# Kernel optimization log

Hardware: AMD Instinct MI355X
Metric: run time of the kernel (lower is better)

## Reference

```python
import jax, jax.numpy as jnp
import numpy as np

NB, T, N, C = 8, 8, 6890, 128
CLASS_NUM = 7
D_SUM = 512
PCADIM = 64
V = 7702  # garment template vertex count
EPS = 1e-5


def setup_inputs() -> dict:
    key = jax.random.key(0)
    ks = jax.random.split(key, 12)
    f = lambda k, s: jax.random.normal(k, s, dtype=jnp.float32)
    return {
        "x": f(ks[0], (NB, T, N, 3)),
        "sem_logits": f(ks[1], (NB * T, N, CLASS_NUM)),
        "feature": f(ks[2], (NB * T, C, N)),
        "garment_summary": f(ks[3], (NB, T, D_SUM)),
        "W1": f(ks[4], (128, D_SUM)) * 0.02, "b1": jnp.zeros((128,), jnp.float32),
        "g1": jnp.ones((128,), jnp.float32), "be1": jnp.zeros((128,), jnp.float32),
        "rm1": jnp.zeros((128,), jnp.float32), "rv1": jnp.ones((128,), jnp.float32),
        "W2": f(ks[5], (64, 128)) * 0.02, "b2": jnp.zeros((64,), jnp.float32),
        "g2": jnp.ones((64,), jnp.float32), "be2": jnp.zeros((64,), jnp.float32),
        "rm2": jnp.zeros((64,), jnp.float32), "rv2": jnp.ones((64,), jnp.float32),
        "W3": f(ks[6], (PCADIM, 64)) * 0.02, "b3": jnp.zeros((PCADIM,), jnp.float32),
        "pca_comp": f(ks[7], (PCADIM, V * 3)) * 0.02,
        "pca_mean": f(ks[8], (V * 3,)) * 0.02,
        "pca_scale": jnp.abs(f(ks[9], (V * 3,))) + 0.5,
        "garment_label": 1,
        "n": N // 4,
    }


def _segmentation_gather(x, sem_logits, feature, garment_label, n):
    # Vectorized form of the per-sample boolean-mask select / truncate / zero-pad loop.
    # x: [B,N,3]; feature: [B,C,N]; sem_logits: [B,N,K]
    feat = jnp.swapaxes(feature, 1, 2)                     # [B,N,C]
    labels = jnp.argmax(sem_logits, axis=2)                # [B,N] (detached in original)
    mask = labels == garment_label                         # [B,N]
    count = mask.sum(axis=1)                               # [B]
    # stable argsort puts selected (mask=True -> key False=0) indices first, in order
    order = jnp.argsort(jnp.logical_not(mask), axis=1)[:, :n]   # [B,n]
    valid = (jnp.arange(n)[None, :] < count[:, None]).astype(x.dtype)  # [B,n]
    gv = jnp.take_along_axis(x, order[:, :, None], axis=1) * valid[:, :, None]
    gf = jnp.take_along_axis(feat, order[:, :, None], axis=1) * valid[:, :, None]
    return gv, gf


def reference(x, sem_logits, feature, garment_summary, W1, b1, g1, be1, rm1, rv1,
              W2, b2, g2, be2, rm2, rv2, W3, b3, pca_comp, pca_mean, pca_scale,
              garment_label, n):
    nbatch, t = x.shape[0], x.shape[1]
    xf = x.reshape(nbatch * t, -1, 3)
    garment_v, garment_f = _segmentation_gather(xf, sem_logits, feature, garment_label, n)

    # PCAEncoder: 1x1 Conv1d over a length-1 sequence == linear layers; BN in eval mode
    def bn(h, g, be, rm, rv):
        return (h - rm) * jax.lax.rsqrt(rv + EPS) * g + be

    gs = garment_summary.max(axis=1)                       # [nbatch, 512] (max over T)
    h = jax.nn.relu(bn(gs @ W1.T + b1, g1, be1, rm1, rv1))
    h = jax.nn.relu(bn(h @ W2.T + b2, g2, be2, rm2, rv2))
    coeff = h @ W3.T + b3                                  # [nbatch, PCADIM]

    # PCA_inverse_transform
    tpose = ((coeff @ pca_comp) + pca_mean) * pca_scale
    tpose = tpose.reshape(coeff.shape[0], -1, 3)           # [nbatch, V, 3]
    return garment_v, garment_f, coeff, tpose
```

## Files before the change

kernel.cpp:

```cpp
#include <hip/hip_runtime.h>

#define NBATCH   8
#define TT       8
#define NPTS     6890
#define KCLS     7
#define CCH      128
#define BSAMP    64
#define NOUT     1722
#define DSUM     512
#define PCADIM   64
#define V3       23106
#define EPSBN    1e-5f

#define NW       108
#define PCH      64
#define LDSP     129
#define CPG      6
#define NGRP     18
#define K4B      91
#define NGATHER  (BSAMP * NGRP)

#define OFF_GV     0
#define OFF_GF     (BSAMP * NOUT * 3)
#define OFF_COEFF  (OFF_GF + BSAMP * NOUT * CCH)
#define OFF_TPOSE  (OFF_COEFF + NBATCH * PCADIM)

__global__ __launch_bounds__(256) void k_prep(
    const float* __restrict__ logits,
    const int*   __restrict__ d_label,
    const float* __restrict__ x,
    unsigned long long* __restrict__ ws_mask,
    float* __restrict__ gv,
    int*   __restrict__ ws_spref,
    int*   __restrict__ ws_count,
    const float* __restrict__ gsum,
    const float* __restrict__ W1, const float* __restrict__ b1,
    const float* __restrict__ g1, const float* __restrict__ be1,
    const float* __restrict__ rm1, const float* __restrict__ rv1,
    const float* __restrict__ W2, const float* __restrict__ b2,
    const float* __restrict__ g2, const float* __restrict__ be2,
    const float* __restrict__ rm2, const float* __restrict__ rv2,
    const float* __restrict__ W3, const float* __restrict__ b3,
    float* __restrict__ coeff_out, float* __restrict__ coeff_ws)
{
    const int tid = threadIdx.x;

    if (blockIdx.x < BSAMP) {
        const int b = blockIdx.x;
        const int label = d_label[0];
        __shared__ unsigned long long smask[NW];
        __shared__ int spref[NW + 1];

        const float* lb = logits + (size_t)b * NPTS * KCLS;
        #pragma unroll 1
        for (int r = 0; r < 27; ++r) {
            const int i = r * 256 + tid;
            bool sel = false;
            if (i < NPTS) {
                const float* p = lb + (size_t)i * KCLS;
                float best = p[0]; int bi = 0;
                #pragma unroll
                for (int k = 1; k < KCLS; ++k) {
                    float v = p[k];
                    if (v > best) { best = v; bi = k; }
                }
                sel = (bi == label);
            }
            const unsigned long long m = __ballot(sel);
            if ((tid & 63) == 0) {
                const int w = r * 4 + (tid >> 6);
                if (w < NW) smask[w] = m;
            }
        }
        __syncthreads();

        if (tid == 0) {
            int run = 0;
            for (int w = 0; w < NW; ++w) { spref[w] = run; run += __popcll(smask[w]); }
            spref[NW] = run;
            ws_count[b] = run < NOUT ? run : NOUT;
        }
        __syncthreads();
        if (tid < NW) {
            ws_mask [b * NW + tid] = smask[tid];
            ws_spref[b * NW + tid] = spref[tid];
        }

        const float* xb = x + (size_t)b * NPTS * 3;
        for (int i = tid; i < NPTS; i += 256) {
            const int w = i >> 6, lb6 = i & 63;
            const unsigned long long m = smask[w];
            if ((m >> lb6) & 1ull) {
                const int pos = spref[w] + __popcll(m & ((1ull << lb6) - 1ull));
                if (pos < NOUT) {
                    const size_t go = ((size_t)b * NOUT + pos) * 3;
                    gv[go + 0] = xb[(size_t)i * 3 + 0];
                    gv[go + 1] = xb[(size_t)i * 3 + 1];
                    gv[go + 2] = xb[(size_t)i * 3 + 2];
                }
            }
        }

        int cnt = spref[NW]; if (cnt > NOUT) cnt = NOUT;
        for (int j = cnt + tid; j < NOUT; j += 256) {
            float* gp = gv + ((size_t)b * NOUT + j) * 3;
            gp[0] = 0.f; gp[1] = 0.f; gp[2] = 0.f;
        }
    } else {
        const int s    = blockIdx.x - BSAMP;
        const int lane = tid & 63;
        const int wv   = tid >> 6;

        __shared__ float gs[DSUM];
        __shared__ float h1[128];
        __shared__ float h2[64];

        for (int d = tid; d < DSUM; d += 256) {
            const float* p = gsum + ((size_t)s * TT) * DSUM + d;
            float m = p[0];
            #pragma unroll
            for (int t = 1; t < TT; ++t) m = fmaxf(m, p[(size_t)t * DSUM]);
            gs[d] = m;
        }
        __syncthreads();

        for (int r = 0; r < 32; r += 2) {
            const int j0 = wv * 32 + r, j1 = j0 + 1;
            const float* w0 = W1 + (size_t)j0 * DSUM;
            const float* w1 = W1 + (size_t)j1 * DSUM;
            float pa = 0.f, pb = 0.f;
            #pragma unroll
            for (int d = lane; d < DSUM; d += 64) {
                const float gd = gs[d];
                pa = fmaf(w0[d], gd, pa);
                pb = fmaf(w1[d], gd, pb);
            }
            #pragma unroll
            for (int off = 32; off; off >>= 1) {
                pa += __shfl_xor(pa, off);
                pb += __shfl_xor(pb, off);
            }
            if (lane == 0) {
                pa += b1[j0];
                pa = (pa - rm1[j0]) * rsqrtf(rv1[j0] + EPSBN) * g1[j0] + be1[j0];
                h1[j0] = fmaxf(pa, 0.f);
                pb += b1[j1];
                pb = (pb - rm1[j1]) * rsqrtf(rv1[j1] + EPSBN) * g1[j1] + be1[j1];
                h1[j1] = fmaxf(pb, 0.f);
            }
        }
        __syncthreads();

        for (int r = 0; r < 16; ++r) {
            const int jj = wv * 16 + r;
            const float* w = W2 + (size_t)jj * 128;
            float p = w[lane] * h1[lane] + w[lane + 64] * h1[lane + 64];
            #pragma unroll
            for (int off = 32; off; off >>= 1) p += __shfl_xor(p, off);
            if (lane == 0) {
                p += b2[jj];
                p = (p - rm2[jj]) * rsqrtf(rv2[jj] + EPSBN) * g2[jj] + be2[jj];
                h2[jj] = fmaxf(p, 0.f);
            }
        }
        __syncthreads();

        for (int r = 0; r < 16; ++r) {
            const int jj = wv * 16 + r;
            float p = W3[(size_t)jj * 64 + lane] * h2[lane];
            #pragma unroll
            for (int off = 32; off; off >>= 1) p += __shfl_xor(p, off);
            if (lane == 0) {
                p += b3[jj];
                coeff_out[s * PCADIM + jj] = p;
                coeff_ws[s * PCADIM + jj]  = p;
            }
        }
    }
}

__global__ __launch_bounds__(256, 4) void k_gather(
    const float* __restrict__ feature,
    const unsigned long long* __restrict__ ws_mask,
    const int* __restrict__ ws_spref,
    const int* __restrict__ ws_count,
    float* __restrict__ gf,
    const float* __restrict__ coeff_ws,
    const float* __restrict__ comp,
    const float* __restrict__ mean_,
    const float* __restrict__ scale_,
    float* __restrict__ tpose)
{
    __shared__ float lds[PCH * LDSP];
    __shared__ int   spos[PCH];
    __shared__ int   sel_list[PCH];
    __shared__ int   s_nsel;

    const int tid = threadIdx.x;

    if (blockIdx.x < K4B) {
        float* sc = lds;
        for (int o = tid; o < NBATCH * PCADIM; o += 256) sc[o] = coeff_ws[o];
        __syncthreads();

        const int v = blockIdx.x * 256 + tid;
        if (v >= V3) return;

        float acc[NBATCH];
        #pragma unroll
        for (int s = 0; s < NBATCH; ++s) acc[s] = 0.f;
        for (int k = 0; k < PCADIM; ++k) {
            const float pv = comp[(size_t)k * V3 + v];
            #pragma unroll
            for (int s = 0; s < NBATCH; ++s)
                acc[s] = fmaf(sc[s * PCADIM + k], pv, acc[s]);
        }
        const float mn = mean_[v], scl = scale_[v];
        #pragma unroll
        for (int s = 0; s < NBATCH; ++s)
            tpose[(size_t)s * V3 + v] = (acc[s] + mn) * scl;
        return;
    }

    const int gb  = blockIdx.x - K4B;
    const int b   = gb / NGRP;
    const int g   = gb % NGRP;
    const int pt2 = tid & 31;
    const int cg  = tid >> 5;
    const int p0  = pt2 * 2;
    const float* fbase = feature + (size_t)b * CCH * NPTS;

    float2 rc[16], rn[16];

    {
        const int i0 = g * (CPG * PCH);
        const int il = min(PCH, NPTS - i0);
        const float* fb = fbase + i0 + p0;
        if (p0 < il) {
            #pragma unroll
            for (int it = 0; it < 16; ++it)
                rc[it] = *(const float2*)(fb + (size_t)(cg + 8 * it) * NPTS);
        } else {
            #pragma unroll
            for (int it = 0; it < 16; ++it) rc[it] = make_float2(0.f, 0.f);
        }
    }

    {
        const int cnt  = ws_count[b];
        const int tail = NOUT - cnt;
        if (tail > 0) {
            const int share = (tail + NGRP - 1) / NGRP;
            const int r0    = cnt + g * share;
            const int r1    = min(r0 + share, NOUT);
            const int nrows = r1 - r0;
            if (nrows > 0) {
                float4* base4 = (float4*)(gf + ((size_t)b * NOUT + r0) * CCH);
                const int total = nrows * 32;
                for (int f = tid; f < total; f += 256)
                    base4[f] = make_float4(0.f, 0.f, 0.f, 0.f);
            }
        }
    }

    #pragma unroll
    for (int c = 0; c < CPG; ++c) {
        const int chunk = g * CPG + c;

        if (c + 1 < CPG) {
            const int i1 = (chunk + 1) * PCH;
            const int il = min(PCH, NPTS - i1);
            const float* fb = fbase + i1 + p0;
            if (p0 < il) {
                #pragma unroll
                for (int it = 0; it < 16; ++it)
                    rn[it] = *(const float2*)(fb + (size_t)(cg + 8 * it) * NPTS);
            } else {
                #pragma unroll
                for (int it = 0; it < 16; ++it) rn[it] = make_float2(0.f, 0.f);
            }
        }

        __syncthreads();

        #pragma unroll
        for (int it = 0; it < 16; ++it) {
            const int cch = cg + 8 * it;
            lds[p0 * LDSP + cch]       = rc[it].x;
            lds[(p0 + 1) * LDSP + cch] = rc[it].y;
        }

        if (tid < 64) {
            const unsigned long long m = ws_mask[b * NW + chunk];
            const int base = ws_spref[b * NW + chunk];
            const int sel  = (int)((m >> tid) & 1ull);
            const int pos  = base + __popcll(m & ((1ull << tid) - 1ull));
            const int sp   = (sel && pos < NOUT) ? pos : -1;
            spos[tid] = sp;
            const unsigned long long mm = __ballot(sp >= 0);
            const int before = __popcll(mm & ((1ull << tid) - 1ull));
            if (sp >= 0) sel_list[before] = tid;
            if (tid == 0) s_nsel = __popcll(mm);
        }
        __syncthreads();

        const int nsel = s_nsel;
        const int cc = tid & 127;
        for (int s = tid >> 7; s < nsel; s += 2) {
            const int p = sel_list[s];
            gf[((size_t)b * NOUT + spos[p]) * CCH + cc] = lds[p * LDSP + cc];
        }

        if (c + 1 < CPG) {
            #pragma unroll
            for (int it = 0; it < 16; ++it) rc[it] = rn[it];
        }
    }
}

extern "C" void kernel_launch(void* const* d_in, const int* in_sizes, int n_in,
                              void* d_out, int out_size, void* d_ws, size_t ws_size,
                              hipStream_t stream) {
    const float* x      = (const float*)d_in[0];
    const float* logits = (const float*)d_in[1];
    const float* feat   = (const float*)d_in[2];
    const float* gsum   = (const float*)d_in[3];
    const float* W1  = (const float*)d_in[4];
    const float* b1  = (const float*)d_in[5];
    const float* g1  = (const float*)d_in[6];
    const float* be1 = (const float*)d_in[7];
    const float* rm1 = (const float*)d_in[8];
    const float* rv1 = (const float*)d_in[9];
    const float* W2  = (const float*)d_in[10];
    const float* b2  = (const float*)d_in[11];
    const float* g2  = (const float*)d_in[12];
    const float* be2 = (const float*)d_in[13];
    const float* rm2 = (const float*)d_in[14];
    const float* rv2 = (const float*)d_in[15];
    const float* W3  = (const float*)d_in[16];
    const float* b3  = (const float*)d_in[17];
    const float* comp  = (const float*)d_in[18];
    const float* mean_ = (const float*)d_in[19];
    const float* scale_= (const float*)d_in[20];
    const int* d_label = (const int*)d_in[21];

    float* out   = (float*)d_out;
    float* gv    = out + OFF_GV;
    float* gf    = out + OFF_GF;
    float* coeff = out + OFF_COEFF;
    float* tpose = out + OFF_TPOSE;

    unsigned long long* ws_mask = (unsigned long long*)d_ws;
    int*   ws_spref = (int*)(ws_mask + BSAMP * NW);
    int*   ws_count = ws_spref + BSAMP * NW;
    float* coeff_ws = (float*)(ws_count + BSAMP);

    k_prep  <<<BSAMP + NBATCH,  256, 0, stream>>>(logits, d_label, x, ws_mask, gv,
                                                  ws_spref, ws_count,
                                                  gsum, W1, b1, g1, be1, rm1, rv1,
                                                  W2, b2, g2, be2, rm2, rv2, W3, b3,
                                                  coeff, coeff_ws);
    k_gather<<<K4B + NGATHER,   256, 0, stream>>>(feat, ws_mask, ws_spref, ws_count,
                                                  gf, coeff_ws, comp, mean_, scale_,
                                                  tpose);
}
```

Measured before the change: 99.07 us.

## Retile gather blocks to 128-point chunks with split channel halves

Each gather block now covers 128 points by 64 channels instead of 64 points by all 128 channels. Channels are split into two halves across blocks, so the total block count stays the same. Each wave now reads a contiguous 512-byte span of a feature row, and the shared-memory tile is transposed so reads during the scatter avoid bank conflicts. The trade-off is that each output row is written as two 256-byte half-rows from different blocks rather than one 512-byte row.

Result: faster. 92.03 us (-7.1%).

```diff
diff --git a/kernel.cpp b/kernel.cpp
--- a/kernel.cpp
+++ b/kernel.cpp
@@ -13,12 +13,15 @@
 #define EPSBN    1e-5f
 
 #define NW       108
-#define PCH      64
-#define LDSP     129
+#define PCH      128
+#define NCHK     54
+#define CHB      2
+#define CHN      64
+#define LDSQ     129
 #define CPG      6
-#define NGRP     18
+#define NGRP     9
 #define K4B      91
-#define NGATHER  (BSAMP * NGRP)
+#define NGATHER  (BSAMP * CHB * NGRP)
 
 #define OFF_GV     0
 #define OFF_GF     (BSAMP * NOUT * 3)
@@ -191,10 +194,10 @@
     const float* __restrict__ scale_,
     float* __restrict__ tpose)
 {
-    __shared__ float lds[PCH * LDSP];
+    __shared__ float lds[CHN * LDSQ];
     __shared__ int   spos[PCH];
     __shared__ int   sel_list[PCH];
-    __shared__ int   s_nsel;
+    __shared__ int   s_ns[2];
 
     const int tid = threadIdx.x;
 
@@ -223,12 +226,15 @@
     }
 
     const int gb  = blockIdx.x - K4B;
-    const int b   = gb / NGRP;
-    const int g   = gb % NGRP;
-    const int pt2 = tid & 31;
-    const int cg  = tid >> 5;
-    const int p0  = pt2 * 2;
-    const float* fbase = feature + (size_t)b * CCH * NPTS;
+    const int b   = gb / (CHB * NGRP);
+    const int rem = gb % (CHB * NGRP);
+    const int cb  = rem / NGRP;
+    const int g   = rem % NGRP;
+
+    const int lane = tid & 63;
+    const int cg   = tid >> 6;
+    const int p0   = lane * 2;
+    const float* fbase = feature + ((size_t)b * CCH + cb * CHN) * NPTS;
 
     float2 rc[16], rn[16];
 
@@ -239,7 +245,7 @@
         if (p0 < il) {
             #pragma unroll
             for (int it = 0; it < 16; ++it)
-                rc[it] = *(const float2*)(fb + (size_t)(cg + 8 * it) * NPTS);
+                rc[it] = *(const float2*)(fb + (size_t)(cg * 16 + it) * NPTS);
         } else {
             #pragma unroll
             for (int it = 0; it < 16; ++it) rc[it] = make_float2(0.f, 0.f);
@@ -250,8 +256,10 @@
         const int cnt  = ws_count[b];
         const int tail = NOUT - cnt;
         if (tail > 0) {
-            const int share = (tail + NGRP - 1) / NGRP;
-            const int r0    = cnt + g * share;
+            const int nshares = CHB * NGRP;
+            const int share = (tail + nshares - 1) / nshares;
+            const int idx   = cb * NGRP + g;
+            const int r0    = cnt + idx * share;
             const int r1    = min(r0 + share, NOUT);
             const int nrows = r1 - r0;
             if (nrows > 0) {
@@ -274,7 +282,7 @@
             if (p0 < il) {
                 #pragma unroll
                 for (int it = 0; it < 16; ++it)
-                    rn[it] = *(const float2*)(fb + (size_t)(cg + 8 * it) * NPTS);
+                    rn[it] = *(const float2*)(fb + (size_t)(cg * 16 + it) * NPTS);
             } else {
                 #pragma unroll
                 for (int it = 0; it < 16; ++it) rn[it] = make_float2(0.f, 0.f);
@@ -285,30 +293,37 @@
 
         #pragma unroll
         for (int it = 0; it < 16; ++it) {
-            const int cch = cg + 8 * it;
-            lds[p0 * LDSP + cch]       = rc[it].x;
-            lds[(p0 + 1) * LDSP + cch] = rc[it].y;
-        }
-
-        if (tid < 64) {
-            const unsigned long long m = ws_mask[b * NW + chunk];
-            const int base = ws_spref[b * NW + chunk];
-            const int sel  = (int)((m >> tid) & 1ull);
-            const int pos  = base + __popcll(m & ((1ull << tid) - 1ull));
+            const int cch = cg * 16 + it;
+            lds[cch * LDSQ + p0]     = rc[it].x;
+            lds[cch * LDSQ + p0 + 1] = rc[it].y;
+        }
+
+        if (tid < 128) {
+            const int w    = tid >> 6;
+            const int word = 2 * chunk + w;
+            const unsigned long long m = ws_mask[b * NW + word];
+            const int base = ws_spref[b * NW + word];
+            const int sel  = (int)((m >> lane) & 1ull);
+            const int pos  = base + __popcll(m & ((1ull << lane) - 1ull));
             const int sp   = (sel && pos < NOUT) ? pos : -1;
             spos[tid] = sp;
             const unsigned long long mm = __ballot(sp >= 0);
-            const int before = __popcll(mm & ((1ull << tid) - 1ull));
-            if (sp >= 0) sel_list[before] = tid;
-            if (tid == 0) s_nsel = __popcll(mm);
-        }
-        __syncthreads();
-
-        const int nsel = s_nsel;
-        const int cc = tid & 127;
-        for (int s = tid >> 7; s < nsel; s += 2) {
-            const int p = sel_list[s];
-            gf[((size_t)b * NOUT + spos[p]) * CCH + cc] = lds[p * LDSP + cc];
+            const int before = __popcll(mm & ((1ull << lane) - 1ull));
+            if (sp >= 0) sel_list[w * 64 + before] = tid;
+            if (lane == 0) s_ns[w] = __popcll(mm);
+        }
+        __syncthreads();
+
+        const int rw = tid >> 6;
+        #pragma unroll 1
+        for (int w = 0; w < 2; ++w) {
+            const int ns = s_ns[w];
+            for (int s = rw; s < ns; s += 4) {
+                const int p   = sel_list[w * 64 + s];
+                const int pos = spos[p];
+                gf[((size_t)b * NOUT + pos) * CCH + cb * CHN + lane] =
+                    lds[lane * LDSQ + p];
+            }
         }
 
         if (c + 1 < CPG) {
```
